# Optimization experiments

Hardware: AMD Instinct MI355X
Metric: run time of the kernel (lower is better)

Reference implementation:

```python
import jax, jax.numpy as jnp
import numpy as np

B, S, D = 4, 2048, 512
H, DH = 8, 64          # heads, dim_head; inner_dim = H*DH = D
QN, QP = -128, 127     # signed 8-bit range (LSQ, all_positive=False)
UQP = 255              # unsigned 8-bit range for softmax output

# scale-vector layout (one learnable LSQ scale per quantizer, as in the module)
# 0:s_hs 1:s_a_q 2:s_w_q 3:s_a_k 4:s_w_k 5:s_a_v 6:s_w_v
# 7:s_qk_a 8:s_qk_b 9:s_softmax 10:s_av_a 11:s_av_b 12:s_a_out 13:s_w_out

def fq(x, s, qn=QN, qp=QP):
    """LSQ fake quantization: clamp(round(x/s), qn, qp) * s, STE on round."""
    v = jnp.clip(x / s, qn, qp)
    vq = v + jax.lax.stop_gradient(jnp.round(v) - v)
    return vq * s


def setup_inputs() -> dict:
    key = jax.random.key(0)
    ks = jax.random.split(key, 6)
    hs = jax.random.normal(ks[0], (B, S, D), dtype=jnp.float32)
    w_std = 0.02
    Wq = jax.random.normal(ks[1], (D, D), dtype=jnp.float32) * w_std
    Wk = jax.random.normal(ks[2], (D, D), dtype=jnp.float32) * w_std
    Wv = jax.random.normal(ks[3], (D, D), dtype=jnp.float32) * w_std
    Wo = jax.random.normal(ks[4], (D, D), dtype=jnp.float32) * w_std
    bo = jnp.zeros((D,), dtype=jnp.float32)
    scales = jnp.array([
        0.03,    # s_hs: hs ~ N(0,1), clip at ~4 sigma
        0.03, 0.001,   # to_q act / weight
        0.03, 0.001,   # to_k act / weight
        0.03, 0.001,   # to_v act / weight
        0.02, 0.02,    # mul_qk a/b
        1.0 / 255.0,   # softmax output (unsigned)
        1.0 / 255.0, 0.02,  # mul_av a/b
        0.01, 0.001,   # to_out act / weight
    ], dtype=jnp.float32)
    return {"hs": hs, "Wq": Wq, "Wk": Wk, "Wv": Wv, "Wo": Wo, "bo": bo,
            "scales": scales}


def reference(hs, Wq, Wk, Wv, Wo, bo, scales):
    sc = scales
    scale = DH ** (-0.5)
    # quan_hs_before_attn (encoder_hidden_states = hs in self-attention)
    hs_q = fq(hs, sc[0])
    # Linear_Quan: LSQ-quantized activation @ LSQ-quantized weight
    def qlin(x, W, sa, sw):
        return jnp.einsum('bsd,ed->bse', fq(x, sa), fq(W, sw))
    q = qlin(hs_q, Wq, sc[1], sc[2])
    k = qlin(hs_q, Wk, sc[3], sc[4])
    v = qlin(hs_q, Wv, sc[5], sc[6])
    # 'b s (h d) -> b h s d'
    q = q.reshape(B, S, H, DH).transpose(0, 2, 1, 3)
    k = k.reshape(B, S, H, DH).transpose(0, 2, 1, 3)
    v = v.reshape(B, S, H, DH).transpose(0, 2, 1, 3)
    # QuanMMHead(q, k^T): quantize both operands, then matmul
    attn = jnp.einsum('bhsd,bhtd->bhst', fq(q, sc[7]), fq(k, sc[8])) * scale
    # QuanSoftmax: softmax then unsigned 8-bit fake quant of probabilities
    attn = fq(jax.nn.softmax(attn, axis=-1), sc[9], 0, UQP)
    # QuanMMHead(attn, v)
    out = jnp.einsum('bhst,bhtd->bhsd', fq(attn, sc[10]), fq(v, sc[11]))
    # '(b h) s d -> b s (h d)'
    out = out.transpose(0, 2, 1, 3).reshape(B, S, H * DH)
    # to_out[0]: Linear_Quan with bias (dropout is identity in eval)
    out = jnp.einsum('bsd,ed->bse', fq(out, sc[12]), fq(Wo, sc[13])) + bo
    return out
```

## Files before the change

kernel.cpp:

```cpp
#include <hip/hip_runtime.h>

typedef _Float16 half8  __attribute__((ext_vector_type(8)));
typedef float    f32x4  __attribute__((ext_vector_type(4)));
typedef unsigned short ushort8 __attribute__((ext_vector_type(8)));

__device__ __forceinline__ float clampf(float v, float lo, float hi){
    return fminf(fmaxf(v, lo), hi);
}
__device__ __forceinline__ float b2f(unsigned short u){
    unsigned int x = ((unsigned int)u) << 16;
    return __builtin_bit_cast(float, x);
}
__device__ __forceinline__ unsigned short f2b(float f){
    unsigned int u = __builtin_bit_cast(unsigned int, f);
    u += 0x7FFFu + ((u >> 16) & 1u);
    return (unsigned short)(u >> 16);
}
__device__ __forceinline__ float fexp2(float x){ return __builtin_amdgcn_exp2f(x); }

__device__ __forceinline__ void gld_lds16(const _Float16* g, _Float16* lds_uniform){
    __builtin_amdgcn_global_load_lds(
        (const __attribute__((address_space(1))) void*)g,
        (__attribute__((address_space(3))) void*)lds_uniform, 16, 0, 0);
}

#define EW_WALL 0u
#define EW_WO   786432u
#define EW_AQ   1048576u
#define EW_AK   (EW_AQ + 4194304u)
#define EW_AV   (EW_AK + 4194304u)
#define EW_Q    (EW_AV + 4194304u)
#define EW_K    (EW_Q  + 4194304u)
#define EW_VT   (EW_K  + 4194304u)
#define EW_O    (EW_VT + 4194304u)

__global__ __launch_bounds__(256) void k_quant_w(
    const unsigned short* __restrict__ Wq, const unsigned short* __restrict__ Wk,
    const unsigned short* __restrict__ Wv, const unsigned short* __restrict__ Wo,
    _Float16* __restrict__ w_all, _Float16* __restrict__ wo16,
    const unsigned short* __restrict__ scu)
{
    int gid  = blockIdx.x * 256 + threadIdx.x;
    int idx8 = gid * 8;
    int which = idx8 >> 18;
    int rem   = idx8 & 262143;
    const unsigned short* W = (which==0)? Wq : (which==1)? Wk : (which==2)? Wv : Wo;
    float sw = b2f((which<3) ? scu[2 + 2*which] : scu[13]);
    ushort8 w = *(const ushort8*)(W + rem);
    half8 o;
    #pragma unroll
    for (int j=0;j<8;j++)
        o[j] = (_Float16)rintf(clampf(b2f(w[j])/sw, -128.f, 127.f));
    _Float16* dst = (which<3) ? (w_all + which*262144 + rem) : (wo16 + rem);
    *(half8*)dst = o;
}

__global__ __launch_bounds__(256) void k_quant_a(
    const unsigned short* __restrict__ hs,
    _Float16* __restrict__ aq, _Float16* __restrict__ ak, _Float16* __restrict__ av,
    const unsigned short* __restrict__ scu)
{
    int gid = blockIdx.x * 256 + threadIdx.x;
    int i8 = gid * 8;
    float s0 = b2f(scu[0]), s1 = b2f(scu[1]), s3 = b2f(scu[3]), s5 = b2f(scu[5]);
    ushort8 h = *(const ushort8*)(hs + i8);
    half8 q, k, v;
    #pragma unroll
    for (int j=0;j<8;j++){
        float h1 = rintf(clampf(b2f(h[j])/s0, -128.f, 127.f)) * s0;
        q[j] = (_Float16)rintf(clampf(h1/s1, -128.f, 127.f));
        k[j] = (_Float16)rintf(clampf(h1/s3, -128.f, 127.f));
        v[j] = (_Float16)rintf(clampf(h1/s5, -128.f, 127.f));
    }
    *(half8*)(aq+i8) = q;
    *(half8*)(ak+i8) = k;
    *(half8*)(av+i8) = v;
}

__global__ __launch_bounds__(256) void k_gemm_qkv(
    const _Float16* __restrict__ aq, const _Float16* __restrict__ ak,
    const _Float16* __restrict__ av, const _Float16* __restrict__ w_all,
    _Float16* __restrict__ q16, _Float16* __restrict__ k16, _Float16* __restrict__ vt16,
    const unsigned short* __restrict__ scu)
{
    __shared__ __align__(16) union SMem {
        struct { _Float16 At[128][64]; _Float16 Bt[64][64]; } ab;
        _Float16 Vt[64][132];
    } sm;
    int tid = threadIdx.x;
    int m0 = blockIdx.x*128, n0 = blockIdx.y*64;
    int proj = blockIdx.y >> 3;
    const _Float16* Ag = (proj==0)? aq : (proj==1)? ak : av;
    int w = tid>>6, lane = tid&63, l15 = lane&15, quad = lane>>4;
    int wm = w>>1, wn = w&1;
    f32x4 z = {0.f,0.f,0.f,0.f};
    f32x4 acc[4][2];
    #pragma unroll
    for (int i=0;i<4;i++)
      #pragma unroll
      for (int j=0;j<2;j++) acc[i][j] = z;

    for (int k0=0; k0<512; k0+=64){
        #pragma unroll
        for (int it=0; it<4; it++){
            int idx = it*256 + tid;
            int row = idx>>3, col = (idx&7)*8;
            int ubase = (it*256 + w*64)*8;
            gld_lds16(Ag + (m0+row)*512 + k0 + col, &sm.ab.At[0][0] + ubase);
        }
        #pragma unroll
        for (int it=0; it<2; it++){
            int idx = it*256 + tid;
            int row = idx>>3, col = (idx&7)*8;
            int ubase = (it*256 + w*64)*8;
            gld_lds16(w_all + (n0+row)*512 + k0 + col, &sm.ab.Bt[0][0] + ubase);
        }
        __syncthreads();
        half8 af[4][2], bf[2][2];
        #pragma unroll
        for (int mt=0; mt<4; mt++){
            af[mt][0] = *(const half8*)(&sm.ab.At[wm*64+mt*16+l15][quad*8]);
            af[mt][1] = *(const half8*)(&sm.ab.At[wm*64+mt*16+l15][32+quad*8]);
        }
        #pragma unroll
        for (int nt=0; nt<2; nt++){
            bf[nt][0] = *(const half8*)(&sm.ab.Bt[wn*32+nt*16+l15][quad*8]);
            bf[nt][1] = *(const half8*)(&sm.ab.Bt[wn*32+nt*16+l15][32+quad*8]);
        }
        #pragma unroll
        for (int mt=0; mt<4; mt++)
          #pragma unroll
          for (int nt=0; nt<2; nt++){
            acc[mt][nt] = __builtin_amdgcn_mfma_f32_16x16x32_f16(af[mt][0], bf[nt][0], acc[mt][nt], 0,0,0);
            acc[mt][nt] = __builtin_amdgcn_mfma_f32_16x16x32_f16(af[mt][1], bf[nt][1], acc[mt][nt], 0,0,0);
          }
        __syncthreads();
    }

    float ssc = b2f(scu[1+2*proj]) * b2f(scu[2+2*proj]);
    float qs  = b2f((proj==0)? scu[7] : (proj==1)? scu[8] : scu[11]);
    if (proj < 2){
        #pragma unroll
        for (int mt=0; mt<4; mt++){
          #pragma unroll
          for (int nt=0; nt<2; nt++){
            int n = n0 + wn*32 + nt*16 + l15;
            int nloc = n & 511;
            int h = nloc>>6, d = nloc&63;
            #pragma unroll
            for (int r=0;r<4;r++){
              int m = m0 + wm*64 + mt*16 + quad*4 + r;
              int b = m>>11, s = m&2047;
              int bh = b*8 + h;
              float val = acc[mt][nt][r] * ssc;
              float qv = rintf(clampf(val/qs, -128.f, 127.f));
              if (proj==0) q16[(bh*2048 + s)*64 + d] = (_Float16)qv;
              else         k16[(bh*2048 + s)*64 + d] = (_Float16)qv;
            }
          }
        }
    } else {
        #pragma unroll
        for (int mt=0; mt<4; mt++){
          #pragma unroll
          for (int nt=0; nt<2; nt++){
            int nl = wn*32 + nt*16 + l15;
            #pragma unroll
            for (int r=0;r<4;r++){
              int ml = wm*64 + mt*16 + quad*4 + r;
              float val = acc[mt][nt][r] * ssc;
              sm.Vt[nl][ml] = (_Float16)rintf(clampf(val/qs, -128.f, 127.f));
            }
          }
        }
        __syncthreads();
        int vrow = tid >> 2;
        int vcol = (tid & 3) * 32;
        int nloc2 = (n0 & 511) + vrow;
        int h2 = nloc2 >> 6, d2 = nloc2 & 63;
        int bh2 = (m0 >> 11)*8 + h2;
        int s2 = (m0 & 2047) + vcol;
        _Float16* dst = vt16 + (bh2*64 + d2)*2048 + s2;
        #pragma unroll
        for (int i=0;i<4;i++)
            *(half8*)(dst + i*8) = *(const half8*)(&sm.Vt[vrow][vcol + i*8]);
    }
}

__global__ __launch_bounds__(256, 5) void k_attn(
    const _Float16* __restrict__ q16, const _Float16* __restrict__ k16,
    const _Float16* __restrict__ vt16, _Float16* __restrict__ o16,
    const unsigned short* __restrict__ scu)
{
    __shared__ __align__(16) _Float16 Kbuf[2][64][72];
    __shared__ __align__(16) _Float16 p16[4][16][72];
    int tid = threadIdx.x;
    int w = tid>>6, lane = tid&63, l15 = lane&15, quad = lane>>4;
    int bh = blockIdx.y;
    int q0 = blockIdx.x*64 + w*16;
    float s9 = b2f(scu[9]), s10 = b2f(scu[10]);
    float al2 = b2f(scu[7]) * b2f(scu[8]) * 0.125f * 1.44269504088896341f;

    f32x4 z = {0.f,0.f,0.f,0.f};
    const _Float16* qr = q16 + (bh*2048 + q0 + l15)*64;
    half8 aq0 = *(const half8*)(qr + quad*8);
    half8 aq1 = *(const half8*)(qr + 32 + quad*8);

    const _Float16* kg    = k16  + bh*131072;
    const _Float16* vbase = vt16 + bh*131072;
    int srow = tid>>3, scol = (tid&7)*8;

    half8 kst[2];
    #pragma unroll
    for (int i=0;i<2;i++) kst[i] = *(const half8*)(kg + i*2048 + tid*8);

    float l[4] = {0.f, 0.f, 0.f, 0.f};
    float cmx[32];

    #pragma unroll
    for (int ch=0; ch<32; ch++){
        int buf = ch & 1;
        #pragma unroll
        for (int i=0;i<2;i++) *(half8*)(&Kbuf[buf][srow + i*32][scol]) = kst[i];
        __syncthreads();
        if (ch < 31){
            const _Float16* nsrc = kg + (ch+1)*4096;
            #pragma unroll
            for (int i=0;i<2;i++) kst[i] = *(const half8*)(nsrc + i*2048 + tid*8);
        }
        f32x4 s[4];
        #pragma unroll
        for (int j=0;j<4;j++){
            half8 bk0 = *(const half8*)(&Kbuf[buf][j*16+l15][quad*8]);
            half8 bk1 = *(const half8*)(&Kbuf[buf][j*16+l15][32+quad*8]);
            f32x4 t = __builtin_amdgcn_mfma_f32_16x16x32_f16(aq0, bk0, z, 0,0,0);
            s[j]    = __builtin_amdgcn_mfma_f32_16x16x32_f16(aq1, bk1, t, 0,0,0);
        }
        float mx = s[0][0];
        #pragma unroll
        for (int j=0;j<4;j++){
            #pragma unroll
            for (int r=0;r<4;r++){
                mx = fmaxf(mx, s[j][r]);
                l[r] += fexp2(s[j][r]*al2);
            }
        }
        cmx[ch] = mx;
    }

    #pragma unroll
    for (int r=0;r<4;r++){
        #pragma unroll
        for (int d=1; d<16; d<<=1)
            l[r] += __shfl_xor(l[r], d, 64);
    }
    float inv_s9 = 1.0f / s9;
    float r910   = s9 / s10;
    float lq9[4];
    #pragma unroll
    for (int r=0;r<4;r++) lq9[r] = log2f(inv_s9 / l[r]);
    float lm = fmaxf(fmaxf(lq9[0], lq9[1]), fmaxf(lq9[2], lq9[3]));
    lm = fmaxf(lm, __shfl_xor(lm, 16, 64));
    lm = fmaxf(lm, __shfl_xor(lm, 32, 64));
    unsigned int mask = 0u;
    #pragma unroll
    for (int ch=0; ch<32; ch++){
        float cm = cmx[ch];
        #pragma unroll
        for (int d=1; d<64; d<<=1) cm = fmaxf(cm, __shfl_xor(cm, d, 64));
        if (fmaf(cm, al2, lm) > -1.0001f) mask |= (1u << ch);
    }

    f32x4 oacc[4];
    #pragma unroll
    for (int dt=0; dt<4; dt++) oacc[dt] = z;
    for (int ch=0; ch<32; ch++){
        if (!(mask & (1u << ch))) continue;
        const _Float16* kc = kg + ch*4096;
        f32x4 s[4];
        #pragma unroll
        for (int j=0;j<4;j++){
            const _Float16* kr = kc + (j*16+l15)*64;
            half8 bk0 = *(const half8*)(kr + quad*8);
            half8 bk1 = *(const half8*)(kr + 32 + quad*8);
            f32x4 t = __builtin_amdgcn_mfma_f32_16x16x32_f16(aq0, bk0, z, 0,0,0);
            s[j]    = __builtin_amdgcn_mfma_f32_16x16x32_f16(aq1, bk1, t, 0,0,0);
        }
        float av[4][4];
        float amax = 0.f;
        #pragma unroll
        for (int j=0;j<4;j++){
            #pragma unroll
            for (int r=0;r<4;r++){
                float p1i = rintf(fminf(fexp2(fmaf(s[j][r], al2, lq9[r])), 255.f));
                float a   = rintf(fminf(p1i*r910, 127.f));
                av[j][r] = a;
                amax = fmaxf(amax, a);
            }
        }
        if (__ballot(amax > 0.f)){
            #pragma unroll
            for (int j=0;j<4;j++)
                #pragma unroll
                for (int r=0;r<4;r++)
                    p16[w][quad*4+r][j*16+l15] = (_Float16)av[j][r];
            half8 ap0 = *(const half8*)(&p16[w][l15][quad*8]);
            half8 ap1 = *(const half8*)(&p16[w][l15][32+quad*8]);
            #pragma unroll
            for (int dt=0; dt<4; dt++){
                const _Float16* vr0 = vbase + (dt*16+l15)*2048 + ch*64;
                half8 b0 = *(const half8*)(vr0 + quad*8);
                half8 b1 = *(const half8*)(vr0 + 32 + quad*8);
                oacc[dt] = __builtin_amdgcn_mfma_f32_16x16x32_f16(ap0, b0, oacc[dt], 0,0,0);
                oacc[dt] = __builtin_amdgcn_mfma_f32_16x16x32_f16(ap1, b1, oacc[dt], 0,0,0);
            }
        }
    }

    float s1011 = b2f(scu[10]) * b2f(scu[11]);
    float s12   = b2f(scu[12]);
    int b = bh>>3, h = bh&7;
    #pragma unroll
    for (int dt=0; dt<4; dt++){
        #pragma unroll
        for (int r=0;r<4;r++){
            float o = oacc[dt][r] * s1011;
            _Float16 v = (_Float16)rintf(clampf(o/s12, -128.f, 127.f));
            o16[(b*2048 + q0 + quad*4 + r)*512 + h*64 + dt*16 + l15] = v;
        }
    }
}

__global__ __launch_bounds__(256) void k_gemm_out(
    const _Float16* __restrict__ o16, const _Float16* __restrict__ wo16,
    const unsigned short* __restrict__ bo, unsigned short* __restrict__ out,
    const unsigned short* __restrict__ scu)
{
    __shared__ __align__(16) _Float16 At[64][64];
    __shared__ __align__(16) _Float16 Bt[64][64];
    int tid = threadIdx.x;
    int m0 = blockIdx.x*64, n0 = blockIdx.y*64;
    int w = tid>>6, lane = tid&63, l15 = lane&15, quad = lane>>4;
    int wm = w>>1, wn = w&1;
    f32x4 z = {0.f,0.f,0.f,0.f};
    f32x4 acc[2][2];
    #pragma unroll
    for (int i=0;i<2;i++)
      #pragma unroll
      for (int j=0;j<2;j++) acc[i][j] = z;

    for (int k0=0; k0<512; k0+=64){
        #pragma unroll
        for (int it=0; it<2; it++){
            int idx = it*256 + tid;
            int row = idx>>3, col = (idx&7)*8;
            int ubase = (it*256 + w*64)*8;
            gld_lds16(o16  + (m0+row)*512 + k0 + col, &At[0][0] + ubase);
        }
        #pragma unroll
        for (int it=0; it<2; it++){
            int idx = it*256 + tid;
            int row = idx>>3, col = (idx&7)*8;
            int ubase = (it*256 + w*64)*8;
            gld_lds16(wo16 + (n0+row)*512 + k0 + col, &Bt[0][0] + ubase);
        }
        __syncthreads();
        half8 af[2][2], bf[2][2];
        #pragma unroll
        for (int mt=0; mt<2; mt++){
            af[mt][0] = *(const half8*)(&At[wm*32+mt*16+l15][quad*8]);
            af[mt][1] = *(const half8*)(&At[wm*32+mt*16+l15][32+quad*8]);
        }
        #pragma unroll
        for (int nt=0; nt<2; nt++){
            bf[nt][0] = *(const half8*)(&Bt[wn*32+nt*16+l15][quad*8]);
            bf[nt][1] = *(const half8*)(&Bt[wn*32+nt*16+l15][32+quad*8]);
        }
        #pragma unroll
        for (int mt=0; mt<2; mt++)
          #pragma unroll
          for (int nt=0; nt<2; nt++){
            acc[mt][nt] = __builtin_amdgcn_mfma_f32_16x16x32_f16(af[mt][0], bf[nt][0], acc[mt][nt], 0,0,0);
            acc[mt][nt] = __builtin_amdgcn_mfma_f32_16x16x32_f16(af[mt][1], bf[nt][1], acc[mt][nt], 0,0,0);
          }
        __syncthreads();
    }

    float ssc = b2f(scu[12]) * b2f(scu[13]);
    #pragma unroll
    for (int mt=0; mt<2; mt++){
      #pragma unroll
      for (int nt=0; nt<2; nt++){
        int n = n0 + wn*32 + nt*16 + l15;
        float bn = b2f(bo[n]);
        #pragma unroll
        for (int r=0;r<4;r++){
          int m = m0 + wm*32 + mt*16 + quad*4 + r;
          out[m*512 + n] = f2b(acc[mt][nt][r]*ssc + bn);
        }
      }
    }
}

extern "C" void kernel_launch(void* const* d_in, const int* in_sizes, int n_in,
                              void* d_out, int out_size, void* d_ws, size_t ws_size,
                              hipStream_t stream)
{
    const unsigned short* hs = (const unsigned short*)d_in[0];
    const unsigned short* Wq = (const unsigned short*)d_in[1];
    const unsigned short* Wk = (const unsigned short*)d_in[2];
    const unsigned short* Wv = (const unsigned short*)d_in[3];
    const unsigned short* Wo = (const unsigned short*)d_in[4];
    const unsigned short* bo = (const unsigned short*)d_in[5];
    const unsigned short* sc = (const unsigned short*)d_in[6];
    unsigned short* out = (unsigned short*)d_out;

    _Float16* wsh   = (_Float16*)d_ws;
    _Float16* w_all = wsh + EW_WALL;
    _Float16* wo16  = wsh + EW_WO;
    _Float16* a_q   = wsh + EW_AQ;
    _Float16* a_k   = wsh + EW_AK;
    _Float16* a_v   = wsh + EW_AV;
    _Float16* q16   = wsh + EW_Q;
    _Float16* k16   = wsh + EW_K;
    _Float16* vt16  = wsh + EW_VT;
    _Float16* o16   = wsh + EW_O;

    k_quant_w<<<512,  256, 0, stream>>>(Wq, Wk, Wv, Wo, w_all, wo16, sc);
    k_quant_a<<<2048, 256, 0, stream>>>(hs, a_q, a_k, a_v, sc);
    k_gemm_qkv<<<dim3(64,24), 256, 0, stream>>>(a_q, a_k, a_v, w_all, q16, k16, vt16, sc);
    k_attn<<<dim3(32,32), 256, 0, stream>>>(q16, k16, vt16, o16, sc);
    k_gemm_out<<<dim3(128,8), 256, 0, stream>>>(o16, wo16, bo, out, sc);
}
```

Before: 174.5 us.

## Split attention normalizer pass into a key-split kernel and merge quant kernels

Moves the first attention pass (softmax denominator and per-chunk max) into a separate kernel that splits the keys four ways, launching 4096 blocks instead of 1024. Partial sums and chunk maxima go to workspace and are combined in the PV kernel. The two quantization kernels are merged into one launch. This raises parallelism for the sum pass and removes a launch, at the cost of an extra kernel boundary, global round trips for the partials, and a reload of Q in the second kernel.

```diff
diff --git a/kernel.cpp b/kernel.cpp
--- a/kernel.cpp
+++ b/kernel.cpp
@@ -34,47 +34,46 @@
 #define EW_VT   (EW_K  + 4194304u)
 #define EW_O    (EW_VT + 4194304u)
 
-__global__ __launch_bounds__(256) void k_quant_w(
+__global__ __launch_bounds__(256) void k_quant(
+    const unsigned short* __restrict__ hs,
     const unsigned short* __restrict__ Wq, const unsigned short* __restrict__ Wk,
     const unsigned short* __restrict__ Wv, const unsigned short* __restrict__ Wo,
     _Float16* __restrict__ w_all, _Float16* __restrict__ wo16,
-    const unsigned short* __restrict__ scu)
-{
-    int gid  = blockIdx.x * 256 + threadIdx.x;
-    int idx8 = gid * 8;
-    int which = idx8 >> 18;
-    int rem   = idx8 & 262143;
-    const unsigned short* W = (which==0)? Wq : (which==1)? Wk : (which==2)? Wv : Wo;
-    float sw = b2f((which<3) ? scu[2 + 2*which] : scu[13]);
-    ushort8 w = *(const ushort8*)(W + rem);
-    half8 o;
-    #pragma unroll
-    for (int j=0;j<8;j++)
-        o[j] = (_Float16)rintf(clampf(b2f(w[j])/sw, -128.f, 127.f));
-    _Float16* dst = (which<3) ? (w_all + which*262144 + rem) : (wo16 + rem);
-    *(half8*)dst = o;
-}
-
-__global__ __launch_bounds__(256) void k_quant_a(
-    const unsigned short* __restrict__ hs,
     _Float16* __restrict__ aq, _Float16* __restrict__ ak, _Float16* __restrict__ av,
     const unsigned short* __restrict__ scu)
 {
-    int gid = blockIdx.x * 256 + threadIdx.x;
-    int i8 = gid * 8;
-    float s0 = b2f(scu[0]), s1 = b2f(scu[1]), s3 = b2f(scu[3]), s5 = b2f(scu[5]);
-    ushort8 h = *(const ushort8*)(hs + i8);
-    half8 q, k, v;
-    #pragma unroll
-    for (int j=0;j<8;j++){
-        float h1 = rintf(clampf(b2f(h[j])/s0, -128.f, 127.f)) * s0;
-        q[j] = (_Float16)rintf(clampf(h1/s1, -128.f, 127.f));
-        k[j] = (_Float16)rintf(clampf(h1/s3, -128.f, 127.f));
-        v[j] = (_Float16)rintf(clampf(h1/s5, -128.f, 127.f));
-    }
-    *(half8*)(aq+i8) = q;
-    *(half8*)(ak+i8) = k;
-    *(half8*)(av+i8) = v;
+    int blk = blockIdx.x;
+    if (blk < 512){
+        int gid  = blk * 256 + threadIdx.x;
+        int idx8 = gid * 8;
+        int which = idx8 >> 18;
+        int rem   = idx8 & 262143;
+        const unsigned short* W = (which==0)? Wq : (which==1)? Wk : (which==2)? Wv : Wo;
+        float sw = b2f((which<3) ? scu[2 + 2*which] : scu[13]);
+        ushort8 w = *(const ushort8*)(W + rem);
+        half8 o;
+        #pragma unroll
+        for (int j=0;j<8;j++)
+            o[j] = (_Float16)rintf(clampf(b2f(w[j])/sw, -128.f, 127.f));
+        _Float16* dst = (which<3) ? (w_all + which*262144 + rem) : (wo16 + rem);
+        *(half8*)dst = o;
+    } else {
+        int gid = (blk - 512) * 256 + threadIdx.x;
+        int i8 = gid * 8;
+        float s0 = b2f(scu[0]), s1 = b2f(scu[1]), s3 = b2f(scu[3]), s5 = b2f(scu[5]);
+        ushort8 h = *(const ushort8*)(hs + i8);
+        half8 q, k, v;
+        #pragma unroll
+        for (int j=0;j<8;j++){
+            float h1 = rintf(clampf(b2f(h[j])/s0, -128.f, 127.f)) * s0;
+            q[j] = (_Float16)rintf(clampf(h1/s1, -128.f, 127.f));
+            k[j] = (_Float16)rintf(clampf(h1/s3, -128.f, 127.f));
+            v[j] = (_Float16)rintf(clampf(h1/s5, -128.f, 127.f));
+        }
+        *(half8*)(aq+i8) = q;
+        *(half8*)(ak+i8) = k;
+        *(half8*)(av+i8) = v;
+    }
 }
 
 __global__ __launch_bounds__(256) void k_gemm_qkv(
@@ -187,17 +186,98 @@
     }
 }
 
-__global__ __launch_bounds__(256, 5) void k_attn(
+__global__ __launch_bounds__(256, 6) void k_attn_l(
     const _Float16* __restrict__ q16, const _Float16* __restrict__ k16,
-    const _Float16* __restrict__ vt16, _Float16* __restrict__ o16,
+    float* __restrict__ lpart, float* __restrict__ cmxg,
     const unsigned short* __restrict__ scu)
 {
     __shared__ __align__(16) _Float16 Kbuf[2][64][72];
+    int tid = threadIdx.x;
+    int w = tid>>6, lane = tid&63, l15 = lane&15, quad = lane>>4;
+    int blk = blockIdx.x;
+    int bh = blk >> 7, qg = (blk >> 2) & 31, tq = blk & 3;
+    int q0 = qg*64 + w*16;
+    float al2 = b2f(scu[7]) * b2f(scu[8]) * 0.125f * 1.44269504088896341f;
+
+    f32x4 z = {0.f,0.f,0.f,0.f};
+    const _Float16* qr = q16 + (bh*2048 + q0 + l15)*64;
+    half8 aq0 = *(const half8*)(qr + quad*8);
+    half8 aq1 = *(const half8*)(qr + 32 + quad*8);
+
+    const _Float16* kg = k16 + bh*131072 + tq*32768;
+    int srow = tid>>3, scol = (tid&7)*8;
+
+    half8 kst[2];
+    #pragma unroll
+    for (int i=0;i<2;i++) kst[i] = *(const half8*)(kg + i*2048 + tid*8);
+
+    float l[4] = {0.f, 0.f, 0.f, 0.f};
+    float cmx[8];
+
+    #pragma unroll
+    for (int ch=0; ch<8; ch++){
+        int buf = ch & 1;
+        #pragma unroll
+        for (int i=0;i<2;i++) *(half8*)(&Kbuf[buf][srow + i*32][scol]) = kst[i];
+        __syncthreads();
+        if (ch < 7){
+            const _Float16* nsrc = kg + (ch+1)*4096;
+            #pragma unroll
+            for (int i=0;i<2;i++) kst[i] = *(const half8*)(nsrc + i*2048 + tid*8);
+        }
+        f32x4 s[4];
+        #pragma unroll
+        for (int j=0;j<4;j++){
+            half8 bk0 = *(const half8*)(&Kbuf[buf][j*16+l15][quad*8]);
+            half8 bk1 = *(const half8*)(&Kbuf[buf][j*16+l15][32+quad*8]);
+            f32x4 t = __builtin_amdgcn_mfma_f32_16x16x32_f16(aq0, bk0, z, 0,0,0);
+            s[j]    = __builtin_amdgcn_mfma_f32_16x16x32_f16(aq1, bk1, t, 0,0,0);
+        }
+        float mx = s[0][0];
+        #pragma unroll
+        for (int j=0;j<4;j++){
+            #pragma unroll
+            for (int r=0;r<4;r++){
+                mx = fmaxf(mx, s[j][r]);
+                l[r] += fexp2(s[j][r]*al2);
+            }
+        }
+        cmx[ch] = mx;
+    }
+
+    #pragma unroll
+    for (int r=0;r<4;r++){
+        #pragma unroll
+        for (int d=1; d<16; d<<=1)
+            l[r] += __shfl_xor(l[r], d, 64);
+    }
+    if (l15 == 0){
+        #pragma unroll
+        for (int r=0;r<4;r++)
+            lpart[tq*65536 + bh*2048 + q0 + quad*4 + r] = l[r];
+    }
+    int qt = qg*4 + w;
+    #pragma unroll
+    for (int ch=0; ch<8; ch++){
+        float cm = cmx[ch];
+        #pragma unroll
+        for (int d=1; d<64; d<<=1) cm = fmaxf(cm, __shfl_xor(cm, d, 64));
+        if (lane == 0) cmxg[(bh*128 + qt)*32 + tq*8 + ch] = cm;
+    }
+}
+
+__global__ __launch_bounds__(256, 5) void k_attn_pv(
+    const _Float16* __restrict__ q16, const _Float16* __restrict__ k16,
+    const _Float16* __restrict__ vt16, const float* __restrict__ lpart,
+    const float* __restrict__ cmxg, _Float16* __restrict__ o16,
+    const unsigned short* __restrict__ scu)
+{
     __shared__ __align__(16) _Float16 p16[4][16][72];
     int tid = threadIdx.x;
     int w = tid>>6, lane = tid&63, l15 = lane&15, quad = lane>>4;
     int bh = blockIdx.y;
     int q0 = blockIdx.x*64 + w*16;
+    int qt = blockIdx.x*4 + w;
     float s9 = b2f(scu[9]), s10 = b2f(scu[10]);
     float al2 = b2f(scu[7]) * b2f(scu[8]) * 0.125f * 1.44269504088896341f;
 
@@ -206,70 +286,28 @@
     half8 aq0 = *(const half8*)(qr + quad*8);
     half8 aq1 = *(const half8*)(qr + 32 + quad*8);
 
-    const _Float16* kg    = k16  + bh*131072;
-    const _Float16* vbase = vt16 + bh*131072;
-    int srow = tid>>3, scol = (tid&7)*8;
-
-    half8 kst[2];
-    #pragma unroll
-    for (int i=0;i<2;i++) kst[i] = *(const half8*)(kg + i*2048 + tid*8);
-
-    float l[4] = {0.f, 0.f, 0.f, 0.f};
-    float cmx[32];
-
-    #pragma unroll
-    for (int ch=0; ch<32; ch++){
-        int buf = ch & 1;
-        #pragma unroll
-        for (int i=0;i<2;i++) *(half8*)(&Kbuf[buf][srow + i*32][scol]) = kst[i];
-        __syncthreads();
-        if (ch < 31){
-            const _Float16* nsrc = kg + (ch+1)*4096;
-            #pragma unroll
-            for (int i=0;i<2;i++) kst[i] = *(const half8*)(nsrc + i*2048 + tid*8);
-        }
-        f32x4 s[4];
-        #pragma unroll
-        for (int j=0;j<4;j++){
-            half8 bk0 = *(const half8*)(&Kbuf[buf][j*16+l15][quad*8]);
-            half8 bk1 = *(const half8*)(&Kbuf[buf][j*16+l15][32+quad*8]);
-            f32x4 t = __builtin_amdgcn_mfma_f32_16x16x32_f16(aq0, bk0, z, 0,0,0);
-            s[j]    = __builtin_amdgcn_mfma_f32_16x16x32_f16(aq1, bk1, t, 0,0,0);
-        }
-        float mx = s[0][0];
-        #pragma unroll
-        for (int j=0;j<4;j++){
-            #pragma unroll
-            for (int r=0;r<4;r++){
-                mx = fmaxf(mx, s[j][r]);
-                l[r] += fexp2(s[j][r]*al2);
-            }
-        }
-        cmx[ch] = mx;
-    }
-
-    #pragma unroll
-    for (int r=0;r<4;r++){
-        #pragma unroll
-        for (int d=1; d<16; d<<=1)
-            l[r] += __shfl_xor(l[r], d, 64);
-    }
     float inv_s9 = 1.0f / s9;
     float r910   = s9 / s10;
     float lq9[4];
     #pragma unroll
-    for (int r=0;r<4;r++) lq9[r] = log2f(inv_s9 / l[r]);
+    for (int r=0;r<4;r++){
+        int idx = bh*2048 + q0 + quad*4 + r;
+        float ltot = lpart[idx] + lpart[65536+idx] + lpart[131072+idx] + lpart[196608+idx];
+        lq9[r] = log2f(inv_s9 / ltot);
+    }
     float lm = fmaxf(fmaxf(lq9[0], lq9[1]), fmaxf(lq9[2], lq9[3]));
     lm = fmaxf(lm, __shfl_xor(lm, 16, 64));
     lm = fmaxf(lm, __shfl_xor(lm, 32, 64));
+
+    const float* cmb = cmxg + (bh*128 + qt)*32;
     unsigned int mask = 0u;
     #pragma unroll
     for (int ch=0; ch<32; ch++){
-        float cm = cmx[ch];
-        #pragma unroll
-        for (int d=1; d<64; d<<=1) cm = fmaxf(cm, __shfl_xor(cm, d, 64));
-        if (fmaf(cm, al2, lm) > -1.0001f) mask |= (1u << ch);
-    }
+        if (fmaf(cmb[ch], al2, lm) > -1.0001f) mask |= (1u << ch);
+    }
+
+    const _Float16* kg    = k16  + bh*131072;
+    const _Float16* vbase = vt16 + bh*131072;
 
     f32x4 oacc[4];
     #pragma unroll
@@ -425,10 +463,13 @@
     _Float16* k16   = wsh + EW_K;
     _Float16* vt16  = wsh + EW_VT;
     _Float16* o16   = wsh + EW_O;
-
-    k_quant_w<<<512,  256, 0, stream>>>(Wq, Wk, Wv, Wo, w_all, wo16, sc);
-    k_quant_a<<<2048, 256, 0, stream>>>(hs, a_q, a_k, a_v, sc);
+    float*    lpart = (float*)(wsh + EW_AQ);
+    float*    cmxg  = (float*)(wsh + EW_AQ + 524288u);
+
+    k_quant<<<2560, 256, 0, stream>>>(hs, Wq, Wk, Wv, Wo, w_all, wo16,
+                                      a_q, a_k, a_v, sc);
     k_gemm_qkv<<<dim3(64,24), 256, 0, stream>>>(a_q, a_k, a_v, w_all, q16, k16, vt16, sc);
-    k_attn<<<dim3(32,32), 256, 0, stream>>>(q16, k16, vt16, o16, sc);
+    k_attn_l<<<4096, 256, 0, stream>>>(q16, k16, lpart, cmxg, sc);
+    k_attn_pv<<<dim3(32,32), 256, 0, stream>>>(q16, k16, vt16, lpart, cmxg, o16, sc);
     k_gemm_out<<<dim3(128,8), 256, 0, stream>>>(o16, wo16, bo, out, sc);
 }
```

Measured after the change: 212.8 us. +21.9%, slower.
